# Optimization experiments

Measured on AMD Instinct MI355X. Metric: run time of the kernel, lower is better.

## Reference

```python
import jax, jax.numpy as jnp
import numpy as np

B, T, S_ENC, D = 2, 1024, 1024, 2048
NQ, NKV, H = 16, 8, 256
EPS = 1e-6
CAP = 50.0
SCALE = 0.0625  # query_pre_attn_scalar = head_dim**-0.5
BASE = 10000
K_MASK = -2.3819763e+38


def rms_norm(x, scale, eps=EPS):
    var = jnp.mean(jnp.square(x), axis=-1, keepdims=True)
    return x * jax.lax.rsqrt(var + eps) * (1.0 + scale)


def apply_rope(x, positions, base=BASE):
    # x: [B, L, N, H], positions: [B, L] float. rope_proportion=1.0 -> full head.
    head_dim = x.shape[-1]
    timescale = base ** (2.0 / head_dim * jnp.arange(head_dim // 2, dtype=jnp.float32))
    sinusoid = positions[..., None] / timescale  # [B, L, H/2]
    sinusoid = sinusoid[..., None, :]            # [B, L, 1, H/2]
    sin, cos = jnp.sin(sinusoid), jnp.cos(sinusoid)
    x1, x2 = jnp.split(x, 2, axis=-1)
    return jnp.concatenate([x1 * cos - x2 * sin, x2 * cos + x1 * sin], axis=-1).astype(x.dtype)


def setup_inputs() -> dict:
    key = jax.random.key(0)
    ks = jax.random.split(key, 6)
    hidden_states = jax.random.normal(ks[0], (B, T, D), jnp.float32)
    encoder_hidden_states = jax.random.normal(ks[1], (B, S_ENC, D), jnp.float32)
    position_ids = jnp.broadcast_to(jnp.arange(T, dtype=jnp.int32), (B, T))
    causal = jnp.tril(jnp.ones((T, T), bool))
    merged = jnp.concatenate([causal, jnp.ones((T, S_ENC), bool)], axis=-1)
    merged_attention_mask = jnp.broadcast_to(merged[None, None], (B, 1, T, T + S_ENC))
    q_w = jax.random.normal(ks[2], (NQ, D, H), jnp.float32) * 0.02
    k_w = jax.random.normal(ks[3], (NKV, D, H), jnp.float32) * 0.02
    v_w = jax.random.normal(ks[4], (NKV, D, H), jnp.float32) * 0.02
    o_w = jax.random.normal(ks[5], (NQ, H, D), jnp.float32) * 0.02
    q_scale = jnp.zeros((H,), jnp.float32)
    k_scale = jnp.zeros((H,), jnp.float32)
    return {
        'hidden_states': hidden_states,
        'encoder_hidden_states': encoder_hidden_states,
        'position_ids': position_ids,
        'merged_attention_mask': merged_attention_mask,
        'q_w': q_w, 'k_w': k_w, 'v_w': v_w, 'o_w': o_w,
        'q_scale': q_scale, 'k_scale': k_scale,
    }


def reference(hidden_states, encoder_hidden_states, position_ids, merged_attention_mask,
              q_w, k_w, v_w, o_w, q_scale, k_scale):
    # Fused QKV projections
    q = jnp.einsum('BTD,NDH->BTNH', hidden_states, q_w)
    self_k = jnp.einsum('BTD,NDH->BTNH', hidden_states, k_w)
    self_v = jnp.einsum('BTD,NDH->BTNH', hidden_states, v_w)
    # QK RMSNorm
    q = rms_norm(q, q_scale)
    self_k = rms_norm(self_k, k_scale)
    # RoPE on decoder-side q/k only
    pos = position_ids.astype(jnp.float32)
    q = apply_rope(q, pos)
    self_k = apply_rope(self_k, pos)
    # Cross KV (no RoPE, k-norm applied)
    cross_k = rms_norm(jnp.einsum('BTD,NDH->BTNH', encoder_hidden_states, k_w), k_scale)
    cross_v = jnp.einsum('BTD,NDH->BTNH', encoder_hidden_states, v_w)
    # Merge KV: [B, T+S_enc, NKV, H]
    k = jnp.concatenate([self_k, cross_k], axis=1)
    v = jnp.concatenate([self_v, cross_v], axis=1)
    q = q * SCALE
    # GQA: group query heads over kv heads
    G = NQ // NKV
    qg = q.reshape(B, T, NKV, G, H)
    logits = jnp.einsum('BTKGH,BSKH->BKGTS', qg, k)
    # Logit soft-cap
    logits = CAP * jnp.tanh(logits / CAP)
    mask = merged_attention_mask[:, 0][:, None, None]  # [B,1,1,T,S_comb]
    logits = jnp.where(mask, logits, K_MASK)
    probs = jax.nn.softmax(logits, axis=-1)
    out = jnp.einsum('BKGTS,BSKH->BTKGH', probs, v).reshape(B, T, NQ, H)
    return jnp.einsum('BTNH,NHD->BTD', out, o_w)
```

## Files before the change

### kernel.cpp

```cpp
#include <hip/hip_runtime.h>
#include <hip/hip_bf16.h>
#include <stdint.h>

typedef __hip_bfloat16 bf16;
typedef __attribute__((ext_vector_type(8))) short bv8;
typedef __attribute__((ext_vector_type(4))) float f32x4;


__device__ __forceinline__ f32x4 mfma16(bv8 a, bv8 b, f32x4 c) {
  return __builtin_amdgcn_mfma_f32_16x16x32_bf16(a, b, c, 0, 0, 0);
}

__device__ __forceinline__ void gload16(const void* g, void* lds) {
  __builtin_amdgcn_global_load_lds((const __attribute__((address_space(1))) void*)g,
                                   (__attribute__((address_space(3))) void*)lds, 16, 0, 0);
}

__device__ __forceinline__ void storeC(float* p, float v) { *p = v; }
__device__ __forceinline__ void storeC(bf16* p, float v) { *p = __float2bfloat16(v); }

__global__ void cast_f32_bf16(const float* __restrict__ src, bf16* __restrict__ dst, int n4) {
  int i = blockIdx.x * blockDim.x + threadIdx.x;
  if (i >= n4) return;
  float4 v = reinterpret_cast<const float4*>(src)[i];
  bf16 t[4] = {__float2bfloat16(v.x), __float2bfloat16(v.y),
               __float2bfloat16(v.z), __float2bfloat16(v.w)};
  reinterpret_cast<uint64_t*>(dst)[i] = *reinterpret_cast<uint64_t*>(t);
}

__global__ void transpose_cast(const float* __restrict__ src, bf16* __restrict__ dst,
                               int R, int C) {
  __shared__ float tile[32][33];
  const int z = blockIdx.z;
  const float* s = src + (size_t)z * R * C;
  bf16* d = dst + (size_t)z * R * C;
  const int c0 = blockIdx.x * 32, r0 = blockIdx.y * 32;
  const int x = threadIdx.x, y = threadIdx.y;
#pragma unroll
  for (int i = 0; i < 32; i += 8)
    tile[y + i][x] = s[(size_t)(r0 + y + i) * C + c0 + x];
  __syncthreads();
#pragma unroll
  for (int i = 0; i < 32; i += 8)
    d[(size_t)(c0 + y + i) * R + r0 + x] = __float2bfloat16(tile[x][y + i]);
}

__global__ void transpose_v(const bf16* __restrict__ src, int src_ld,
                            bf16* __restrict__ dst, int t0) {
  __shared__ bf16 tile[32][33];
  const int z = blockIdx.z, b = z >> 3, kvh = z & 7;
  const bf16* s = src + (size_t)(b * 1024) * src_ld + kvh * 256;
  bf16* d = dst + (size_t)(z * 256) * 2048 + t0;
  const int h0 = blockIdx.x * 32, tt0 = blockIdx.y * 32;
  const int x = threadIdx.x, y = threadIdx.y;
#pragma unroll
  for (int i = 0; i < 32; i += 8)
    tile[y + i][x] = s[(size_t)(tt0 + y + i) * src_ld + h0 + x];
  __syncthreads();
#pragma unroll
  for (int i = 0; i < 32; i += 8)
    d[(size_t)(h0 + y + i) * 2048 + tt0 + x] = tile[x][y + i];
}

template <typename CT>
__launch_bounds__(256)
__global__ void gemm_bt(const bf16* __restrict__ A, const bf16* __restrict__ Bt,
                        CT* __restrict__ C, int N, int K) {
  __shared__ __align__(16) bf16 As[128 * 32];
  __shared__ __align__(16) bf16 Bs[128 * 32];
  const int tid = threadIdx.x;
  const int w = tid >> 6, l = tid & 63;
  const int wr = w >> 1, wc = w & 1;
  const int l15 = l & 15, lhi = l >> 4;
  const int m0 = blockIdx.y * 128, n0 = blockIdx.x * 128;
  const bf16* ag = A + (size_t)(m0 + (tid >> 2)) * K + (tid & 3) * 8;
  const bf16* bg = Bt + (size_t)(n0 + (tid >> 2)) * K + (tid & 3) * 8;
  bf16* asw = As + w * 512;
  bf16* bsw = Bs + w * 512;
  f32x4 acc[4][4] = {};
  for (int k0 = 0; k0 < K; k0 += 32) {
    gload16(ag + k0, asw);
    gload16(ag + (size_t)64 * K + k0, asw + 2048);
    gload16(bg + k0, bsw);
    gload16(bg + (size_t)64 * K + k0, bsw + 2048);
    asm volatile("s_waitcnt vmcnt(0)" ::: "memory");
    __syncthreads();
    bv8 af[4], bfv[4];
#pragma unroll
    for (int m = 0; m < 4; ++m)
      af[m] = *reinterpret_cast<const bv8*>(As + (wr * 64 + m * 16 + l15) * 32 + lhi * 8);
#pragma unroll
    for (int n = 0; n < 4; ++n)
      bfv[n] = *reinterpret_cast<const bv8*>(Bs + (wc * 64 + n * 16 + l15) * 32 + lhi * 8);
#pragma unroll
    for (int m = 0; m < 4; ++m)
#pragma unroll
      for (int n = 0; n < 4; ++n)
        acc[m][n] = mfma16(af[m], bfv[n], acc[m][n]);
    __syncthreads();
  }
  const int r0 = m0 + wr * 64 + lhi * 4;
  const int c0 = n0 + wc * 64 + l15;
#pragma unroll
  for (int m = 0; m < 4; ++m)
#pragma unroll
    for (int n = 0; n < 4; ++n) {
      f32x4 v = acc[m][n];
#pragma unroll
      for (int j = 0; j < 4; ++j)
        storeC(&C[(size_t)(r0 + m * 16 + j) * N + c0 + n * 16], v[j]);
    }
}

template <bool ROPE>
__launch_bounds__(256)
__global__ void norm_finalize(const bf16* __restrict__ src, int src_ld, int src_col0,
                              const float* __restrict__ scale,
                              const int* __restrict__ pos_ids,
                              bf16* __restrict__ dst, int nheads, int dst_S, int dst_t0,
                              float mul) {
  const int gid = blockIdx.x * 4 + (threadIdx.x >> 6);
  const int l = threadIdx.x & 63;
  const int token = gid / nheads;
  const int n = gid - token * nheads;
  const int b = token >> 10;
  const int t = token & 1023;
  const size_t soff = (size_t)token * src_ld + src_col0 + n * 256 + l * 4;
  bf16 xb[4];
  *reinterpret_cast<uint64_t*>(xb) = *reinterpret_cast<const uint64_t*>(src + soff);
  float x[4];
#pragma unroll
  for (int c = 0; c < 4; ++c) x[c] = __bfloat162float(xb[c]);
  float ss = x[0] * x[0] + x[1] * x[1] + x[2] * x[2] + x[3] * x[3];
#pragma unroll
  for (int d = 1; d < 64; d <<= 1) ss += __shfl_xor(ss, d);
  const float r = rsqrtf(ss * (1.0f / 256.0f) + 1e-6f);
  float v[4];
#pragma unroll
  for (int c = 0; c < 4; ++c) v[c] = x[c] * r * (1.0f + scale[l * 4 + c]);
  if (ROPE) {
    const float pos = (float)pos_ids[token];
    float o[4];
#pragma unroll
    for (int c = 0; c < 4; ++c) {
      const int j = (l & 31) * 4 + c;
      const float inv_ts = exp2f(-(float)j * 0.10381025296523007f);
      const float arg = pos * inv_ts;
      const float sj = sinf(arg), cj = cosf(arg);
      const float partner = __shfl_xor(v[c], 32);
      o[c] = (l < 32) ? (v[c] * cj - partner * sj) : (v[c] * cj + partner * sj);
    }
#pragma unroll
    for (int c = 0; c < 4; ++c) v[c] = o[c];
  }
  bf16 ob[4];
#pragma unroll
  for (int c = 0; c < 4; ++c) ob[c] = __float2bfloat16(v[c] * mul);
  const size_t doff = ((size_t)((b * nheads + n) * dst_S + dst_t0 + t)) * 256 + l * 4;
  *reinterpret_cast<uint64_t*>(dst + doff) = *reinterpret_cast<uint64_t*>(ob);
}

__launch_bounds__(512, 2)
__global__ void attn_kernel(const bf16* __restrict__ qb, const bf16* __restrict__ kb,
                            const bf16* __restrict__ vt, bf16* __restrict__ attn_out) {
  __shared__ __align__(16) bf16 Ks[2][64 * 256];
  __shared__ __align__(16) bf16 Vs[2][256 * 64];
  __shared__ __align__(16) bf16 pbuf[8][16 * 72];
  const int lin = blockIdx.x + 16 * blockIdx.y;
  const int kvc = (lin & 7) | (((lin >> 7) & 1) << 3);
  const int qt  = (lin >> 3) & 15;
  const int b = kvc >> 3, kvh = kvc & 7;
  const int tid = threadIdx.x, w = tid >> 6, l = tid & 63;
  const int wq = w & 3, g = w >> 2;
  const int n = kvh * 2 + g;
  const int l15 = l & 15, lhi = l >> 4;
  const int xr = (l15 & 7) << 4;

  const bf16* kbase = kb + (size_t)(b * 8 + kvh) * 2048 * 256;
  const bf16* vbase = vt + (size_t)(b * 8 + kvh) * 256 * 2048;

  const bf16* ksrc[4];
  const bf16* vsrc[4];
#pragma unroll
  for (int i = 0; i < 4; ++i) {
    const int r0 = (w * 4 + i) * 2 + (l >> 5);
    const int cbs = ((l & 31) * 16) ^ ((r0 & 7) << 4);
    ksrc[i] = kbase + r0 * 256 + (cbs >> 1);
    const int h0 = (w * 4 + i) * 8 + (l >> 3);
    const int cbv = ((l & 7) * 16) ^ ((h0 & 7) << 4);
    vsrc[i] = vbase + (size_t)h0 * 2048 + (cbv >> 1);
  }

  const bf16* qptr = qb + ((size_t)(b * 16 + n) * 1024 + qt * 64 + wq * 16 + l15) * 256 + lhi * 8;
  bv8 qf[8];
#pragma unroll
  for (int f = 0; f < 8; ++f) qf[f] = *reinterpret_cast<const bv8*>(qptr + f * 32);

  f32x4 oacc[16] = {};
  float rs[4] = {0.f, 0.f, 0.f, 0.f};

  const int nt = qt + 17;

#pragma unroll
  for (int i = 0; i < 4; ++i) gload16(ksrc[i], &Ks[0][(w * 4 + i) * 512]);
#pragma unroll
  for (int i = 0; i < 4; ++i) gload16(vsrc[i], &Vs[0][(w * 4 + i) * 512]);
  asm volatile("s_waitcnt vmcnt(0)" ::: "memory");
  __syncthreads();

  for (int it = 0; it < nt; ++it) {
    const int cur = it & 1;
    if (it + 1 < nt) {
      const int itn = it + 1;
      const int s1 = (itn <= qt) ? itn * 64 : 1024 + (itn - qt - 1) * 64;
#pragma unroll
      for (int i = 0; i < 4; ++i)
        gload16(ksrc[i] + (size_t)s1 * 256, &Ks[cur ^ 1][(w * 4 + i) * 512]);
#pragma unroll
      for (int i = 0; i < 4; ++i)
        gload16(vsrc[i] + s1, &Vs[cur ^ 1][(w * 4 + i) * 512]);
    }
    f32x4 lacc[4] = {};
    __builtin_amdgcn_s_setprio(1);
#pragma unroll
    for (int sub = 0; sub < 4; ++sub) {
      const int rbase = (sub * 16 + l15) * 256;
#pragma unroll
      for (int f = 0; f < 8; ++f) {
        const int off = rbase + (((f * 64 + lhi * 16) ^ xr) >> 1);
        bv8 kf = *reinterpret_cast<const bv8*>(&Ks[cur][off]);
        lacc[sub] = mfma16(qf[f], kf, lacc[sub]);
      }
    }
    __builtin_amdgcn_s_setprio(0);
    const bool diag = (it == qt);
#pragma unroll
    for (int sub = 0; sub < 4; ++sub) {
#pragma unroll
      for (int j = 0; j < 4; ++j) {
        const float raw = lacc[sub][j];
        const float e2 = __expf(raw * 0.04f);
        const bool ok = !diag || (sub * 16 + l15 <= wq * 16 + lhi * 4 + j);
        const float p = ok ? __expf(50.f - __fdividef(100.f, e2 + 1.f)) : 0.f;
        rs[j] += p;
        pbuf[w][(lhi * 4 + j) * 72 + sub * 16 + l15] = __float2bfloat16(p);
      }
    }
    __syncthreads();
    __builtin_amdgcn_s_setprio(1);
#pragma unroll
    for (int ks = 0; ks < 2; ++ks) {
      bv8 pa = *reinterpret_cast<const bv8*>(&pbuf[w][l15 * 72 + ks * 32 + lhi * 8]);
#pragma unroll
      for (int ht = 0; ht < 16; ++ht) {
        const int off = (ht * 16 + l15) * 64 + (((ks * 64 + lhi * 16) ^ xr) >> 1);
        bv8 vf = *reinterpret_cast<const bv8*>(&Vs[cur][off]);
        oacc[ht] = mfma16(pa, vf, oacc[ht]);
      }
    }
    __builtin_amdgcn_s_setprio(0);
    asm volatile("s_waitcnt vmcnt(0)" ::: "memory");
    __syncthreads();
  }
  float invr[4];
#pragma unroll
  for (int j = 0; j < 4; ++j) {
    float s = rs[j];
    s += __shfl_xor(s, 1);
    s += __shfl_xor(s, 2);
    s += __shfl_xor(s, 4);
    s += __shfl_xor(s, 8);
    invr[j] = 1.0f / s;
  }
  bf16* op = attn_out + ((size_t)(b * 1024 + qt * 64 + wq * 16 + lhi * 4) * 4096) + n * 256 + l15;
#pragma unroll
  for (int ht = 0; ht < 16; ++ht)
#pragma unroll
    for (int j = 0; j < 4; ++j)
      op[(size_t)j * 4096 + ht * 16] = __float2bfloat16(oacc[ht][j] * invr[j]);
}

extern "C" void kernel_launch(void* const* d_in, const int* in_sizes, int n_in,
                              void* d_out, int out_size, void* d_ws, size_t ws_size,
                              hipStream_t stream) {
  (void)in_sizes; (void)n_in; (void)out_size; (void)ws_size;
  const float* hidden = (const float*)d_in[0];
  const float* enc    = (const float*)d_in[1];
  const int*   pos    = (const int*)d_in[2];
  const float* q_w = (const float*)d_in[4];
  const float* k_w = (const float*)d_in[5];
  const float* v_w = (const float*)d_in[6];
  const float* o_w = (const float*)d_in[7];
  const float* q_s = (const float*)d_in[8];
  const float* k_s = (const float*)d_in[9];
  float* out = (float*)d_out;

  char* base = (char*)d_ws;
  bf16* hid_b  = (bf16*)(base + 0);
  bf16* enc_b  = (bf16*)(base + 8388608);
  bf16* qb     = (bf16*)(base + 0);
  bf16* wqkvt  = (bf16*)(base + 16777216);
  bf16* kbuf   = (bf16*)(base + 16777216);
  bf16* vtb    = (bf16*)(base + 33554432);
  bf16* owt    = (bf16*)(base + 50331648);
  bf16* cself  = (bf16*)(base + 67108864);
  bf16* attn_b = (bf16*)(base + 67108864);
  bf16* ccross = (bf16*)(base + 100663296);

  dim3 tb32(32, 8);
  cast_f32_bf16<<<4096, 256, 0, stream>>>(hidden, hid_b, 1048576);
  cast_f32_bf16<<<4096, 256, 0, stream>>>(enc, enc_b, 1048576);
  transpose_cast<<<dim3(8, 64, 16), tb32, 0, stream>>>(q_w, wqkvt, 2048, 256);
  transpose_cast<<<dim3(8, 64, 8),  tb32, 0, stream>>>(k_w, wqkvt + 8388608, 2048, 256);
  transpose_cast<<<dim3(8, 64, 8),  tb32, 0, stream>>>(v_w, wqkvt + 12582912, 2048, 256);
  transpose_cast<<<dim3(64, 128, 1), tb32, 0, stream>>>(o_w, owt, 4096, 2048);
  gemm_bt<bf16><<<dim3(64, 16), 256, 0, stream>>>(hid_b, wqkvt, cself, 8192, 2048);
  gemm_bt<bf16><<<dim3(32, 16), 256, 0, stream>>>(enc_b, wqkvt + 8388608, ccross, 4096, 2048);
  norm_finalize<true><<<8192, 256, 0, stream>>>(cself, 8192, 0, q_s, pos, qb, 16, 1024, 0, 0.0625f);
  norm_finalize<true><<<4096, 256, 0, stream>>>(cself, 8192, 4096, k_s, pos, kbuf, 8, 2048, 0, 1.0f);
  norm_finalize<false><<<4096, 256, 0, stream>>>(ccross, 4096, 0, k_s, nullptr, kbuf, 8, 2048, 1024, 1.0f);
  transpose_v<<<dim3(8, 32, 16), tb32, 0, stream>>>(cself + 6144, 8192, vtb, 0);
  transpose_v<<<dim3(8, 32, 16), tb32, 0, stream>>>(ccross + 2048, 4096, vtb, 1024);
  attn_kernel<<<dim3(16, 16), 512, 0, stream>>>(qb, kbuf, vtb, attn_b);
  gemm_bt<float><<<dim3(16, 16), 256, 0, stream>>>(attn_b, owt, out, 2048, 4096);
}
```

Measured before the change: 451.7 us.

## Merge launches, split-K output projection, and drop attention barrier

Result: faster. 376.4 us (-16.7%).

```diff
diff --git a/kernel.cpp b/kernel.cpp
--- a/kernel.cpp
+++ b/kernel.cpp
@@ -19,21 +19,44 @@
 __device__ __forceinline__ void storeC(float* p, float v) { *p = v; }
 __device__ __forceinline__ void storeC(bf16* p, float v) { *p = __float2bfloat16(v); }
 
-__global__ void cast_f32_bf16(const float* __restrict__ src, bf16* __restrict__ dst, int n4) {
+__global__ void cast2_f32_bf16(const float* __restrict__ a, const float* __restrict__ b,
+                               bf16* __restrict__ da, bf16* __restrict__ db, int n4each) {
   int i = blockIdx.x * blockDim.x + threadIdx.x;
-  if (i >= n4) return;
-  float4 v = reinterpret_cast<const float4*>(src)[i];
+  const float* s;
+  bf16* d;
+  if (i < n4each) { s = a; d = da; }
+  else            { s = b; d = db; i -= n4each; }
+  float4 v = reinterpret_cast<const float4*>(s)[i];
   bf16 t[4] = {__float2bfloat16(v.x), __float2bfloat16(v.y),
                __float2bfloat16(v.z), __float2bfloat16(v.w)};
-  reinterpret_cast<uint64_t*>(dst)[i] = *reinterpret_cast<uint64_t*>(t);
+  reinterpret_cast<uint64_t*>(d)[i] = *reinterpret_cast<uint64_t*>(t);
+}
+
+__global__ void transpose_cast_qkv(const float* __restrict__ q_w, const float* __restrict__ k_w,
+                                   const float* __restrict__ v_w, bf16* __restrict__ dst) {
+  __shared__ float tile[32][33];
+  const int z = blockIdx.z;
+  const float* s = (z < 16) ? q_w + (size_t)z * 524288
+                 : (z < 24) ? k_w + (size_t)(z - 16) * 524288
+                            : v_w + (size_t)(z - 24) * 524288;
+  bf16* d = dst + (size_t)z * 524288;
+  const int R = 2048, C = 256;
+  const int c0 = blockIdx.x * 32, r0 = blockIdx.y * 32;
+  const int x = threadIdx.x, y = threadIdx.y;
+#pragma unroll
+  for (int i = 0; i < 32; i += 8)
+    tile[y + i][x] = s[(size_t)(r0 + y + i) * C + c0 + x];
+  __syncthreads();
+#pragma unroll
+  for (int i = 0; i < 32; i += 8)
+    d[(size_t)(c0 + y + i) * R + r0 + x] = __float2bfloat16(tile[x][y + i]);
 }
 
 __global__ void transpose_cast(const float* __restrict__ src, bf16* __restrict__ dst,
                                int R, int C) {
   __shared__ float tile[32][33];
-  const int z = blockIdx.z;
-  const float* s = src + (size_t)z * R * C;
-  bf16* d = dst + (size_t)z * R * C;
+  const float* s = src;
+  bf16* d = dst;
   const int c0 = blockIdx.x * 32, r0 = blockIdx.y * 32;
   const int x = threadIdx.x, y = threadIdx.y;
 #pragma unroll
@@ -45,12 +68,17 @@
     d[(size_t)(c0 + y + i) * R + r0 + x] = __float2bfloat16(tile[x][y + i]);
 }
 
-__global__ void transpose_v(const bf16* __restrict__ src, int src_ld,
-                            bf16* __restrict__ dst, int t0) {
+__global__ void transpose_v2(const bf16* __restrict__ vself, const bf16* __restrict__ vcross,
+                             bf16* __restrict__ dst) {
   __shared__ bf16 tile[32][33];
-  const int z = blockIdx.z, b = z >> 3, kvh = z & 7;
-  const bf16* s = src + (size_t)(b * 1024) * src_ld + kvh * 256;
-  bf16* d = dst + (size_t)(z * 256) * 2048 + t0;
+  const int z = blockIdx.z;
+  const int zz = z & 15, b = zz >> 3, kvh = zz & 7;
+  const bool cross = z >= 16;
+  const bf16* srcb = cross ? vcross : vself;
+  const int src_ld = cross ? 4096 : 8192;
+  const int t0 = cross ? 1024 : 0;
+  const bf16* s = srcb + (size_t)(b * 1024) * src_ld + kvh * 256;
+  bf16* d = dst + (size_t)(zz * 256) * 2048 + t0;
   const int h0 = blockIdx.x * 32, tt0 = blockIdx.y * 32;
   const int x = threadIdx.x, y = threadIdx.y;
 #pragma unroll
@@ -63,22 +91,21 @@
 }
 
 template <typename CT>
-__launch_bounds__(256)
-__global__ void gemm_bt(const bf16* __restrict__ A, const bf16* __restrict__ Bt,
-                        CT* __restrict__ C, int N, int K) {
+__device__ __forceinline__ void gemm_body(const bf16* __restrict__ A, const bf16* __restrict__ Bt,
+                                          CT* __restrict__ C, int N, int K,
+                                          int m0, int n0, int kbase, int ksteps) {
   __shared__ __align__(16) bf16 As[128 * 32];
   __shared__ __align__(16) bf16 Bs[128 * 32];
   const int tid = threadIdx.x;
   const int w = tid >> 6, l = tid & 63;
   const int wr = w >> 1, wc = w & 1;
   const int l15 = l & 15, lhi = l >> 4;
-  const int m0 = blockIdx.y * 128, n0 = blockIdx.x * 128;
-  const bf16* ag = A + (size_t)(m0 + (tid >> 2)) * K + (tid & 3) * 8;
-  const bf16* bg = Bt + (size_t)(n0 + (tid >> 2)) * K + (tid & 3) * 8;
+  const bf16* ag = A + (size_t)(m0 + (tid >> 2)) * K + kbase + (tid & 3) * 8;
+  const bf16* bg = Bt + (size_t)(n0 + (tid >> 2)) * K + kbase + (tid & 3) * 8;
   bf16* asw = As + w * 512;
   bf16* bsw = Bs + w * 512;
   f32x4 acc[4][4] = {};
-  for (int k0 = 0; k0 < K; k0 += 32) {
+  for (int k0 = 0; k0 < ksteps; k0 += 32) {
     gload16(ag + k0, asw);
     gload16(ag + (size_t)64 * K + k0, asw + 2048);
     gload16(bg + k0, bsw);
@@ -110,6 +137,37 @@
       for (int j = 0; j < 4; ++j)
         storeC(&C[(size_t)(r0 + m * 16 + j) * N + c0 + n * 16], v[j]);
     }
+}
+
+__launch_bounds__(256)
+__global__ void gemm_proj(const bf16* __restrict__ hid, const bf16* __restrict__ enc,
+                          const bf16* __restrict__ wqkvt, bf16* __restrict__ cself,
+                          bf16* __restrict__ ccross) {
+  const int bx = blockIdx.x;
+  const bool cross = bx >= 64;
+  const bf16* A = cross ? enc : hid;
+  const bf16* Bt = cross ? wqkvt + 8388608 : wqkvt;
+  bf16* C = cross ? ccross : cself;
+  const int N = cross ? 4096 : 8192;
+  const int n0 = (cross ? bx - 64 : bx) * 128;
+  gemm_body<bf16>(A, Bt, C, N, 2048, blockIdx.y * 128, n0, 0, 2048);
+}
+
+__launch_bounds__(256)
+__global__ void gemm_osplit(const bf16* __restrict__ A, const bf16* __restrict__ Bt,
+                            float* __restrict__ out, float* __restrict__ p1) {
+  float* C = blockIdx.z ? p1 : out;
+  gemm_body<float>(A, Bt, C, 2048, 4096, blockIdx.y * 128, blockIdx.x * 128,
+                   blockIdx.z * 2048, 2048);
+}
+
+__global__ void add_inplace(float* __restrict__ out, const float* __restrict__ p1, int n4) {
+  int i = blockIdx.x * blockDim.x + threadIdx.x;
+  if (i >= n4) return;
+  float4 a = reinterpret_cast<float4*>(out)[i];
+  float4 b = reinterpret_cast<const float4*>(p1)[i];
+  a.x += b.x; a.y += b.y; a.z += b.z; a.w += b.w;
+  reinterpret_cast<float4*>(out)[i] = a;
 }
 
 template <bool ROPE>
@@ -246,7 +304,8 @@
         pbuf[w][(lhi * 4 + j) * 72 + sub * 16 + l15] = __float2bfloat16(p);
       }
     }
-    __syncthreads();
+    asm volatile("s_waitcnt lgkmcnt(0)" ::: "memory");
+    __builtin_amdgcn_sched_barrier(0);
     __builtin_amdgcn_s_setprio(1);
 #pragma unroll
     for (int ks = 0; ks < 2; ++ks) {
@@ -305,22 +364,19 @@
   bf16* owt    = (bf16*)(base + 50331648);
   bf16* cself  = (bf16*)(base + 67108864);
   bf16* attn_b = (bf16*)(base + 67108864);
+  float* p1    = (float*)(base + 83886080);
   bf16* ccross = (bf16*)(base + 100663296);
 
   dim3 tb32(32, 8);
-  cast_f32_bf16<<<4096, 256, 0, stream>>>(hidden, hid_b, 1048576);
-  cast_f32_bf16<<<4096, 256, 0, stream>>>(enc, enc_b, 1048576);
-  transpose_cast<<<dim3(8, 64, 16), tb32, 0, stream>>>(q_w, wqkvt, 2048, 256);
-  transpose_cast<<<dim3(8, 64, 8),  tb32, 0, stream>>>(k_w, wqkvt + 8388608, 2048, 256);
-  transpose_cast<<<dim3(8, 64, 8),  tb32, 0, stream>>>(v_w, wqkvt + 12582912, 2048, 256);
+  cast2_f32_bf16<<<8192, 256, 0, stream>>>(hidden, enc, hid_b, enc_b, 1048576);
+  transpose_cast_qkv<<<dim3(8, 64, 32), tb32, 0, stream>>>(q_w, k_w, v_w, wqkvt);
   transpose_cast<<<dim3(64, 128, 1), tb32, 0, stream>>>(o_w, owt, 4096, 2048);
-  gemm_bt<bf16><<<dim3(64, 16), 256, 0, stream>>>(hid_b, wqkvt, cself, 8192, 2048);
-  gemm_bt<bf16><<<dim3(32, 16), 256, 0, stream>>>(enc_b, wqkvt + 8388608, ccross, 4096, 2048);
+  gemm_proj<<<dim3(96, 16), 256, 0, stream>>>(hid_b, enc_b, wqkvt, cself, ccross);
   norm_finalize<true><<<8192, 256, 0, stream>>>(cself, 8192, 0, q_s, pos, qb, 16, 1024, 0, 0.0625f);
   norm_finalize<true><<<4096, 256, 0, stream>>>(cself, 8192, 4096, k_s, pos, kbuf, 8, 2048, 0, 1.0f);
   norm_finalize<false><<<4096, 256, 0, stream>>>(ccross, 4096, 0, k_s, nullptr, kbuf, 8, 2048, 1024, 1.0f);
-  transpose_v<<<dim3(8, 32, 16), tb32, 0, stream>>>(cself + 6144, 8192, vtb, 0);
-  transpose_v<<<dim3(8, 32, 16), tb32, 0, stream>>>(ccross + 2048, 4096, vtb, 1024);
+  transpose_v2<<<dim3(8, 32, 32), tb32, 0, stream>>>(cself + 6144, ccross + 2048, vtb);
   attn_kernel<<<dim3(16, 16), 512, 0, stream>>>(qb, kbuf, vtb, attn_b);
-  gemm_bt<float><<<dim3(16, 16), 256, 0, stream>>>(attn_b, owt, out, 2048, 4096);
-}
+  gemm_osplit<<<dim3(16, 16, 2), 256, 0, stream>>>(attn_b, owt, out, p1);
+  add_inplace<<<4096, 256, 0, stream>>>(out, p1, 1048576);
+}
```
